# Kernel tuning notes

Hardware: AMD Instinct MI355X
Metric: run time of the kernel (lower is better)

## Reference

```python
import jax, jax.numpy as jnp
import numpy as np

C = 128          # input_channels == output_channels (required by residual + final conv)
MID = C // 4     # hidden width of weight/bias heads
H = W = 64
B = 4
SOFTMAX_SCALE = 1.0


def _leaky(z):
    return jnp.where(z >= 0, z, 0.2 * z)


def _conv1x1(x, w, b):
    # x: [B,Cin,H,W], w: [Cout,Cin], b: [Cout]
    return jnp.einsum('oc,bchw->bohw', w, x) + b[None, :, None, None]


def setup_inputs() -> dict:
    key = jax.random.key(0)
    ks = jax.random.split(key, 16)
    s = 0.05
    inp = {
        'x': jax.random.normal(ks[0], (B, C, H, W), dtype=jnp.float32),
        # 1x1 query / value convs
        'q_w': jax.random.normal(ks[1], (C, C), dtype=jnp.float32) * s,
        'q_b': jnp.zeros((C,), dtype=jnp.float32),
        'v_w': jax.random.normal(ks[2], (C, C), dtype=jnp.float32) * s,
        'v_b': jnp.zeros((C,), dtype=jnp.float32),
        # linear_weight head: conv1x1(C->C/4) -> leaky -> conv1x1(C/4->1)
        'lw1_w': jax.random.normal(ks[3], (MID, C), dtype=jnp.float32) * s,
        'lw1_b': jnp.zeros((MID,), dtype=jnp.float32),
        'lw2_w': jax.random.normal(ks[4], (1, MID), dtype=jnp.float32) * s,
        'lw2_b': jnp.zeros((1,), dtype=jnp.float32),
        # bias head
        'bw1_w': jax.random.normal(ks[5], (MID, C), dtype=jnp.float32) * s,
        'bw1_b': jnp.zeros((MID,), dtype=jnp.float32),
        'bw2_w': jax.random.normal(ks[6], (1, MID), dtype=jnp.float32) * s,
        'bw2_b': jnp.zeros((1,), dtype=jnp.float32),
        # final 3x3 conv (output_channels -> output_channels)
        'lin_w': jax.random.normal(ks[7], (C, C, 3, 3), dtype=jnp.float32) * s,
        'lin_b': jnp.zeros((C,), dtype=jnp.float32),
    }
    return inp


def _attn_sample(q_map, v_map, w_map, b_map):
    # q_map: [C,H,W], v_map: [C,H,W], w_map/b_map: [1,H,W]
    n = H * W
    q = q_map.reshape(C, n)                      # query tokens  [C,N]
    v = v_map.reshape(C, n)                      # value tokens  [C,N]
    w = w_map.reshape(n)
    b = b_map.reshape(n)
    # cosine-normalized keys (normalize each token over channels)
    norm = jnp.sqrt(jnp.sum(q * q, axis=0))      # [N]
    k = q / jnp.clip(norm, 1e-4)[None, :]        # [C,N]
    logits = jnp.einsum('cn,cm->nm', k, q)       # keys x queries [N,N]
    mean = jnp.mean(logits, axis=0, keepdims=True)            # [1,N]
    sparse = jax.nn.relu(logits - mean * w[None, :] + b[None, :])
    mask = (sparse != 0.0).astype(logits.dtype)
    attn = jax.nn.softmax(logits * sparse * SOFTMAX_SCALE, axis=0)
    attn = jnp.clip(attn * mask, 1e-8)
    out = jnp.einsum('cn,nm->cm', v, attn)       # [C,N]
    return out.reshape(C, H, W)


def reference(x, q_w, q_b, v_w, v_b, lw1_w, lw1_b, lw2_w, lw2_b,
              bw1_w, bw1_b, bw2_w, bw2_b, lin_w, lin_b):
    x1 = _conv1x1(x, v_w, v_b)                   # value  [B,C,H,W]
    x2 = _conv1x1(x, q_w, q_b)                   # query  [B,C,H,W]
    weight = _conv1x1(_leaky(_conv1x1(x2, lw1_w, lw1_b)), lw2_w, lw2_b)  # [B,1,H,W]
    bias = _conv1x1(_leaky(_conv1x1(x2, bw1_w, bw1_b)), bw2_w, bw2_b)    # [B,1,H,W]
    y = jax.vmap(_attn_sample)(x2, x1, weight, bias)                      # [B,C,H,W]
    y = jax.lax.conv_general_dilated(
        y, lin_w, window_strides=(1, 1), padding='SAME',
        dimension_numbers=('NCHW', 'OIHW', 'NCHW'))
    y = _leaky(y + lin_b[None, :, None, None])
    return y + x
```

## Files before the change

kernel.cpp:

```cpp
#include <hip/hip_runtime.h>
#include <math.h>

#define BB 4
#define CC 128
#define NN 4096
#define HH 64
#define WW 64
#define YTP 4356

typedef __attribute__((ext_vector_type(8))) short bf16x8;
typedef __attribute__((ext_vector_type(4))) float f32x4;

__device__ inline unsigned short f2bf(float f) {
  unsigned int u = __float_as_uint(f);
  unsigned int r = (u + 0x7FFFu + ((u >> 16) & 1u)) >> 16;
  return (unsigned short)r;
}
__device__ inline float bf2f(short s) {
  union { unsigned u; float f; } x;
  x.u = ((unsigned)(unsigned short)s) << 16;
  return x.f;
}

__global__ __launch_bounds__(256) void xt_kernel(
    const float* __restrict__ x, unsigned short* __restrict__ xtb) {
  int b = blockIdx.y;
  int n0 = blockIdx.x * 64;
  int t = threadIdx.x;
  __shared__ float xs[CC][65];
  for (int l = 0; l < 32; l++) {
    int idx = t + 256 * l;
    int px = idx & 63, c = idx >> 6;
    xs[c][px] = x[((size_t)b * CC + c) * NN + n0 + px];
  }
  __syncthreads();
  int n = t & 63, ch = t >> 6;
  unsigned o[16];
#pragma unroll
  for (int i = 0; i < 32; i += 2) {
    o[i >> 1] = (unsigned)f2bf(xs[32 * ch + i][n]) |
                ((unsigned)f2bf(xs[32 * ch + i + 1][n]) << 16);
  }
  unsigned short* dst = xtb + ((size_t)b * NN + n0 + n) * CC + 32 * ch;
#pragma unroll
  for (int k = 0; k < 4; k++) {
    uint4 v; v.x = o[4 * k]; v.y = o[4 * k + 1]; v.z = o[4 * k + 2]; v.w = o[4 * k + 3];
    *(uint4*)(dst + 8 * k) = v;
  }
}

__global__ __launch_bounds__(256) void wrepack_kernel(
    const float* __restrict__ qw, const float* __restrict__ vw,
    const float* __restrict__ lw1w, const float* __restrict__ bw1w,
    const float* __restrict__ lw, unsigned short* __restrict__ qwb,
    unsigned short* __restrict__ vwb, unsigned short* __restrict__ hwb,
    unsigned short* __restrict__ Wt) {
  int idx = blockIdx.x * 256 + threadIdx.x;
  if (idx < 16384) { qwb[idx] = f2bf(qw[idx]); return; }
  idx -= 16384;
  if (idx < 16384) { vwb[idx] = f2bf(vw[idx]); return; }
  idx -= 16384;
  if (idx < 4096) { hwb[idx] = f2bf(lw1w[idx]); return; }
  idx -= 4096;
  if (idx < 4096) { hwb[4096 + idx] = f2bf(bw1w[idx]); return; }
  idx -= 4096;
  if (idx < CC * 1152) {
    int co = idx / 1152, rem = idx % 1152;
    int tap = rem >> 7, ci = rem & 127;
    Wt[idx] = f2bf(lw[(size_t)(co * CC + ci) * 9 + tap]);
  }
}

__global__ __launch_bounds__(256) void qv_mfma(
    const unsigned short* __restrict__ xtb, const unsigned short* __restrict__ qwb,
    const unsigned short* __restrict__ vwb, const unsigned short* __restrict__ hwb,
    const float* __restrict__ qb, const float* __restrict__ vb,
    const float* __restrict__ lw1b, const float* __restrict__ lw2w,
    const float* __restrict__ lw2b, const float* __restrict__ bw1b,
    const float* __restrict__ bw2w, const float* __restrict__ bw2b,
    unsigned short* __restrict__ qt, unsigned short* __restrict__ qtn,
    float* __restrict__ nrm, float* __restrict__ pSkey,
    unsigned short* __restrict__ vbuf, float* __restrict__ pSumV,
    float* __restrict__ wmap, float* __restrict__ bmap) {
  int b = blockIdx.y;
  int nb = blockIdx.x;
  int n0 = nb * 64;
  int t = threadIdx.x, w = t >> 6, lane = t & 63;
  int col = lane & 15, oct = lane >> 4;
  __shared__ float qs[4][16][132];
  __shared__ float partK[4][128];
  __shared__ float partV[4][128];
  const unsigned short* xb = xtb + (size_t)b * NN * CC;

  f32x4 aq[8], av[8];
#pragma unroll
  for (int i = 0; i < 8; i++) { aq[i] = (f32x4)0.f; av[i] = (f32x4)0.f; }
#pragma unroll
  for (int kc = 0; kc < 4; kc++) {
    bf16x8 Xf = *(const bf16x8*)(xb + (size_t)(n0 + 16 * w + col) * CC + kc * 32 + oct * 8);
#pragma unroll
    for (int ct = 0; ct < 8; ct++) {
      bf16x8 Qf = *(const bf16x8*)(qwb + (16 * ct + col) * CC + kc * 32 + oct * 8);
      aq[ct] = __builtin_amdgcn_mfma_f32_16x16x32_bf16(Xf, Qf, aq[ct], 0, 0, 0);
      bf16x8 Vf = *(const bf16x8*)(vwb + (16 * ct + col) * CC + kc * 32 + oct * 8);
      av[ct] = __builtin_amdgcn_mfma_f32_16x16x32_bf16(Vf, Xf, av[ct], 0, 0, 0);
    }
  }

  unsigned short* vbb = vbuf + (size_t)b * CC * NN;
#pragma unroll
  for (int ct = 0; ct < 8; ct++) {
#pragma unroll
    for (int r = 0; r < 4; r++) {
      int c = 16 * ct + 4 * oct + r;
      float val = av[ct][r] + vb[c];
      vbb[(size_t)c * NN + n0 + 16 * w + col] = f2bf(val);
      float sv = val;
      sv += __shfl_xor(sv, 1); sv += __shfl_xor(sv, 2);
      sv += __shfl_xor(sv, 4); sv += __shfl_xor(sv, 8);
      if (col == 0) partV[w][c] = sv;
    }
  }

#pragma unroll
  for (int ct = 0; ct < 8; ct++) {
#pragma unroll
    for (int r = 0; r < 4; r++) {
      int c = 16 * ct + col;
      qs[w][4 * oct + r][c] = aq[ct][r] + qb[c];
    }
  }
  int row = lane >> 2, cq = (lane & 3) * 32;
  float vals[32];
  float ssq = 0.f;
#pragma unroll
  for (int i = 0; i < 32; i += 4) {
    float4 v4 = *(const float4*)&qs[w][row][cq + i];
    vals[i] = v4.x; vals[i + 1] = v4.y; vals[i + 2] = v4.z; vals[i + 3] = v4.w;
    ssq += v4.x * v4.x + v4.y * v4.y + v4.z * v4.z + v4.w * v4.w;
  }
  ssq += __shfl_xor(ssq, 1); ssq += __shfl_xor(ssq, 2);
  float nm = fmaxf(sqrtf(ssq), 1e-4f), sc = 1.0f / nm;
  int gp = b * NN + n0 + 16 * w + row;
  if ((lane & 3) == 0) nrm[gp] = nm;
  unsigned outq[16], outn[16];
  float sk[32];
#pragma unroll
  for (int i = 0; i < 32; i += 2) {
    unsigned short u0 = f2bf(vals[i]), u1 = f2bf(vals[i + 1]);
    unsigned short m0 = f2bf(vals[i] * sc), m1 = f2bf(vals[i + 1] * sc);
    outq[i >> 1] = (unsigned)u0 | ((unsigned)u1 << 16);
    outn[i >> 1] = (unsigned)m0 | ((unsigned)m1 << 16);
    sk[i] = bf2f((short)m0); sk[i + 1] = bf2f((short)m1);
  }
  unsigned short* qtp = qt + (size_t)gp * CC + cq;
  unsigned short* qnp = qtn + (size_t)gp * CC + cq;
#pragma unroll
  for (int k = 0; k < 4; k++) {
    uint4 v; v.x = outq[4 * k]; v.y = outq[4 * k + 1]; v.z = outq[4 * k + 2]; v.w = outq[4 * k + 3];
    *(uint4*)(qtp + 8 * k) = v;
    uint4 u; u.x = outn[4 * k]; u.y = outn[4 * k + 1]; u.z = outn[4 * k + 2]; u.w = outn[4 * k + 3];
    *(uint4*)(qnp + 8 * k) = u;
  }
#pragma unroll
  for (int i = 0; i < 32; i++) {
    float v = sk[i];
    v += __shfl_xor(v, 4); v += __shfl_xor(v, 8);
    v += __shfl_xor(v, 16); v += __shfl_xor(v, 32);
    if ((lane >> 2) == 0) partK[w][cq + i] = v;
  }

  f32x4 ah[4];
#pragma unroll
  for (int i = 0; i < 4; i++) ah[i] = (f32x4)0.f;
#pragma unroll
  for (int kc = 0; kc < 4; kc++) {
    float4 a0 = *(const float4*)&qs[w][col][kc * 32 + oct * 8];
    float4 a1 = *(const float4*)&qs[w][col][kc * 32 + oct * 8 + 4];
    union { unsigned short s[8]; bf16x8 v; } af;
    af.s[0] = f2bf(a0.x); af.s[1] = f2bf(a0.y); af.s[2] = f2bf(a0.z); af.s[3] = f2bf(a0.w);
    af.s[4] = f2bf(a1.x); af.s[5] = f2bf(a1.y); af.s[6] = f2bf(a1.z); af.s[7] = f2bf(a1.w);
#pragma unroll
    for (int ct = 0; ct < 4; ct++) {
      bf16x8 Bf = *(const bf16x8*)(hwb + (16 * ct + col) * CC + kc * 32 + oct * 8);
      ah[ct] = __builtin_amdgcn_mfma_f32_16x16x32_bf16(af.v, Bf, ah[ct], 0, 0, 0);
    }
  }
  float b1l[2], b1b[2], w2l[2], w2b[2];
#pragma unroll
  for (int ct = 0; ct < 2; ct++) {
    int mid = 16 * ct + col;
    b1l[ct] = lw1b[mid]; w2l[ct] = lw2w[mid];
    b1b[ct] = bw1b[mid]; w2b[ct] = bw2w[mid];
  }
#pragma unroll
  for (int r = 0; r < 4; r++) {
    float wp = 0.f, bp = 0.f;
#pragma unroll
    for (int ct = 0; ct < 2; ct++) {
      float zl = ah[ct][r] + b1l[ct];
      zl = (zl >= 0.f) ? zl : 0.2f * zl;
      wp += w2l[ct] * zl;
      float zb = ah[ct + 2][r] + b1b[ct];
      zb = (zb >= 0.f) ? zb : 0.2f * zb;
      bp += w2b[ct] * zb;
    }
    wp += __shfl_xor(wp, 1); wp += __shfl_xor(wp, 2);
    wp += __shfl_xor(wp, 4); wp += __shfl_xor(wp, 8);
    bp += __shfl_xor(bp, 1); bp += __shfl_xor(bp, 2);
    bp += __shfl_xor(bp, 4); bp += __shfl_xor(bp, 8);
    if (col == 0) {
      int g = b * NN + n0 + 16 * w + 4 * oct + r;
      wmap[g] = wp + lw2b[0];
      bmap[g] = bp + bw2b[0];
    }
  }

  __syncthreads();
  int blk = b * 64 + nb;
  if (t < 128) {
    float s = (partK[0][t] + partK[1][t]) + (partK[2][t] + partK[3][t]);
    pSkey[(size_t)blk * 128 + t] = s;
  } else {
    int c = t - 128;
    float s = (partV[0][c] + partV[1][c]) + (partV[2][c] + partV[3][c]);
    pSumV[(size_t)blk * 128 + c] = s;
  }
}

__global__ __launch_bounds__(256) void reduce_kernel(
    const float* __restrict__ pSkey, const float* __restrict__ pSumV,
    float* __restrict__ Skey, float* __restrict__ SumV) {
  int b = blockIdx.x;
  int t = threadIdx.x;
  const float* src = (t < 128) ? pSkey : pSumV;
  int c = t & 127;
  float s = 0.f;
#pragma unroll 8
  for (int nb = 0; nb < 64; nb++)
    s += src[((size_t)b * 64 + nb) * 128 + c];
  if (t < 128) Skey[b * CC + c] = s;
  else SumV[b * CC + c] = s;
}

__global__ __launch_bounds__(256, 2) void qk_sparse(
    const unsigned short* __restrict__ qt, const unsigned short* __restrict__ qtn,
    const float* __restrict__ nrm, const float* __restrict__ wmap,
    const float* __restrict__ bmap, const float* __restrict__ Skey,
    float* __restrict__ Zacc, unsigned short* __restrict__ Tb,
    int* __restrict__ blist, int* __restrict__ bcnt) {
  int lin = blockIdx.x;
  int mtile = lin >> 6;
  int bks = lin & 63;
  int b = bks >> 4, ks = bks & 15;
  int t = threadIdx.x, wave = t >> 6, lane = t & 63;
  int col = lane & 15, oct = lane >> 4;
  int m0 = mtile * 128 + 32 * wave;
  int bucket = b * 128 + (m0 >> 5);

  __shared__ unsigned short Bt[2][4096];
  __shared__ unsigned short tS[4][32][40];

  const unsigned short* qtb  = qt  + (size_t)b * NN * CC;
  const unsigned short* qtnb = qtn + (size_t)b * NN * CC;

  bf16x8 A[2][4];
#pragma unroll
  for (int mt = 0; mt < 2; mt++)
#pragma unroll
    for (int kc = 0; kc < 4; kc++)
      A[mt][kc] = *(const bf16x8*)(qtb + (size_t)(m0 + 16 * mt + col) * CC + 32 * kc + 8 * oct);

  float stc1[2][4], stzd[2][4];
#pragma unroll
  for (int mt = 0; mt < 2; mt++) {
    float dot = 0.f;
#pragma unroll
    for (int kc = 0; kc < 4; kc++) {
      const float* skp = Skey + b * CC + 32 * kc + 8 * oct;
      float4 s0 = *(const float4*)skp;
      float4 s1 = *(const float4*)(skp + 4);
      bf16x8 a = A[mt][kc];
      dot += bf2f(a[0]) * s0.x + bf2f(a[1]) * s0.y + bf2f(a[2]) * s0.z + bf2f(a[3]) * s0.w;
      dot += bf2f(a[4]) * s1.x + bf2f(a[5]) * s1.y + bf2f(a[6]) * s1.z + bf2f(a[7]) * s1.w;
    }
    dot += __shfl_xor(dot, 16);
    dot += __shfl_xor(dot, 32);
    int m = m0 + 16 * mt + col;
    float c1 = dot * (1.0f / NN) * wmap[(size_t)b * NN + m] - bmap[(size_t)b * NN + m];
    float nm = nrm[(size_t)b * NN + m];
    float zd = nm * fmaxf(nm - c1, 0.f);
#pragma unroll
    for (int r = 0; r < 4; r++) {
      stc1[mt][r] = __shfl(c1, 4 * oct + r);
      stzd[mt][r] = __shfl(zd, 4 * oct + r);
    }
  }

  int n0base = ks * 256;
  {
    int f0 = wave, f1 = wave + 4;
    uint4 r0 = *(const uint4*)(qtnb + (size_t)(n0base + 16 * (f0 >> 2) + col) * CC + (4 * (f0 & 3) + oct) * 8);
    uint4 r1 = *(const uint4*)(qtnb + (size_t)(n0base + 16 * (f1 >> 2) + col) * CC + (4 * (f1 & 3) + oct) * 8);
    *(uint4*)&Bt[0][f0 * 512 + lane * 8] = r0;
    *(uint4*)&Bt[0][f1 * 512 + lane * 8] = r1;
  }
  __syncthreads();

  float zp[2][4];
#pragma unroll
  for (int mt = 0; mt < 2; mt++)
#pragma unroll
    for (int r = 0; r < 4; r++) zp[mt][r] = 0.f;
  bool didwork = false;

  for (int it = 0; it < 8; it++) {
    int cur = it & 1;
    bool more = (it + 1 < 8);
    uint4 r0, r1;
    if (more) {
      int n0n = n0base + (it + 1) * 32;
      int f0 = wave, f1 = wave + 4;
      r0 = *(const uint4*)(qtnb + (size_t)(n0n + 16 * (f0 >> 2) + col) * CC + (4 * (f0 & 3) + oct) * 8);
      r1 = *(const uint4*)(qtnb + (size_t)(n0n + 16 * (f1 >> 2) + col) * CC + (4 * (f1 & 3) + oct) * 8);
    }
    f32x4 acc[2][2];
    acc[0][0] = (f32x4)0.f; acc[0][1] = (f32x4)0.f;
    acc[1][0] = (f32x4)0.f; acc[1][1] = (f32x4)0.f;
#pragma unroll
    for (int nt = 0; nt < 2; nt++)
#pragma unroll
      for (int kc = 0; kc < 4; kc++) {
        bf16x8 Bf = *(const bf16x8*)&Bt[cur][(nt * 4 + kc) * 512 + lane * 8];
        acc[0][nt] = __builtin_amdgcn_mfma_f32_16x16x32_bf16(A[0][kc], Bf, acc[0][nt], 0, 0, 0);
        acc[1][nt] = __builtin_amdgcn_mfma_f32_16x16x32_bf16(A[1][kc], Bf, acc[1][nt], 0, 0, 0);
      }
    float fm = -1e30f;
#pragma unroll
    for (int mt = 0; mt < 2; mt++)
#pragma unroll
      for (int r = 0; r < 4; r++) {
        float lm = fmaxf(acc[mt][0][r], acc[mt][1][r]);
        float ub = fmaxf(lm * fmaxf(lm - stc1[mt][r], 0.f), 0.f);
        fm = fmaxf(fm, ub - stzd[mt][r]);
      }
    if (__any(fm > -18.4207f)) {
      didwork = true;
      int n0 = n0base + it * 32;
#pragma unroll
      for (int mt = 0; mt < 2; mt++)
#pragma unroll
        for (int nt = 0; nt < 2; nt++)
#pragma unroll
          for (int r = 0; r < 4; r++) {
            float l = acc[mt][nt][r];
            float s = l - stc1[mt][r];
            float z = l * fmaxf(s, 0.f);
            float e = __expf(z - stzd[mt][r]);
            zp[mt][r] += e;
            tS[wave][16 * mt + 4 * oct + r][16 * nt + col] = f2bf((s > 0.f) ? e : 0.f);
          }
      int idx;
      if (lane == 0) {
        idx = atomicAdd(&bcnt[bucket], 1);
        if (idx < 128) blist[bucket * 128 + idx] = n0 >> 5;
      }
      idx = __shfl(idx, 0);
      if (idx < 128) {
        const unsigned short* src = &tS[wave][lane >> 1][(lane & 1) * 16];
        unsigned short* dst = Tb + ((size_t)bucket * 128 + idx) * 1024 +
                              (lane >> 1) * 32 + (lane & 1) * 16;
        *(uint4*)dst = *(const uint4*)src;
        *(uint4*)(dst + 8) = *(const uint4*)(src + 8);
      }
    }
    if (more) {
      int nxt = cur ^ 1;
      *(uint4*)&Bt[nxt][wave * 512 + lane * 8] = r0;
      *(uint4*)&Bt[nxt][(wave + 4) * 512 + lane * 8] = r1;
    }
    __syncthreads();
  }

  if (didwork) {
#pragma unroll
    for (int mt = 0; mt < 2; mt++)
#pragma unroll
      for (int r = 0; r < 4; r++) {
        float v = zp[mt][r];
        v += __shfl_xor(v, 1); v += __shfl_xor(v, 2);
        v += __shfl_xor(v, 4); v += __shfl_xor(v, 8);
        if (col == 0)
          atomicAdd(Zacc + (size_t)b * NN + m0 + 16 * mt + 4 * oct + r, v);
      }
  }
}

__global__ __launch_bounds__(1024, 1) void pv_kernel(
    const unsigned short* __restrict__ vb16, const unsigned short* __restrict__ Tb,
    const int* __restrict__ blist, const int* __restrict__ bcnt,
    const float* __restrict__ Zacc, const float* __restrict__ SumV,
    unsigned short* __restrict__ Yt) {
  int bucket = blockIdx.x;
  int b = bucket >> 7;
  int m0 = (bucket & 127) * 32;
  int t = threadIdx.x;
  int w = t >> 6, lane = t & 63;
  int grp = w >> 2, cw = w & 3;
  int col = lane & 15, oct = lane >> 4;
  __shared__ int lst[128];
  __shared__ float red[3][32][132];
  int ntiles = bcnt[bucket];
  if (ntiles > 128) ntiles = 128;
  if (t < ntiles) lst[t] = blist[bucket * 128 + t];
  __syncthreads();
  const unsigned short* Vb = vb16 + (size_t)b * CC * NN;
  const unsigned short* Tbb = Tb + (size_t)bucket * 128 * 1024;

  f32x4 acc[2][2];
  acc[0][0] = (f32x4)0.f; acc[0][1] = (f32x4)0.f;
  acc[1][0] = (f32x4)0.f; acc[1][1] = (f32x4)0.f;

  int nIt = (ntiles > grp) ? ((ntiles - grp + 3) >> 2) : 0;
  bf16x8 B0a, B0b, A0a, A0b, B1a, B1b, A1a, A1b;
  auto ld0 = [&](int idx) {
    int n0 = lst[idx] * 32;
    const unsigned short* Tp = Tbb + (size_t)idx * 1024;
    B0a = *(const bf16x8*)(Tp + col * 32 + 8 * oct);
    B0b = *(const bf16x8*)(Tp + (16 + col) * 32 + 8 * oct);
    A0a = *(const bf16x8*)(Vb + (size_t)(32 * cw + col) * NN + n0 + 8 * oct);
    A0b = *(const bf16x8*)(Vb + (size_t)(32 * cw + 16 + col) * NN + n0 + 8 * oct);
  };
  auto ld1 = [&](int idx) {
    int n0 = lst[idx] * 32;
    const unsigned short* Tp = Tbb + (size_t)idx * 1024;
    B1a = *(const bf16x8*)(Tp + col * 32 + 8 * oct);
    B1b = *(const bf16x8*)(Tp + (16 + col) * 32 + 8 * oct);
    A1a = *(const bf16x8*)(Vb + (size_t)(32 * cw + col) * NN + n0 + 8 * oct);
    A1b = *(const bf16x8*)(Vb + (size_t)(32 * cw + 16 + col) * NN + n0 + 8 * oct);
  };
  if (nIt > 0) ld0(grp);
  for (int k = 0; k < nIt; k += 2) {
    if (k + 1 < nIt) ld1(grp + (k + 1) * 4);
    acc[0][0] = __builtin_amdgcn_mfma_f32_16x16x32_bf16(A0a, B0a, acc[0][0], 0, 0, 0);
    acc[0][1] = __builtin_amdgcn_mfma_f32_16x16x32_bf16(A0a, B0b, acc[0][1], 0, 0, 0);
    acc[1][0] = __builtin_amdgcn_mfma_f32_16x16x32_bf16(A0b, B0a, acc[1][0], 0, 0, 0);
    acc[1][1] = __builtin_amdgcn_mfma_f32_16x16x32_bf16(A0b, B0b, acc[1][1], 0, 0, 0);
    if (k + 1 < nIt) {
      if (k + 2 < nIt) ld0(grp + (k + 2) * 4);
      acc[0][0] = __builtin_amdgcn_mfma_f32_16x16x32_bf16(A1a, B1a, acc[0][0], 0, 0, 0);
      acc[0][1] = __builtin_amdgcn_mfma_f32_16x16x32_bf16(A1a, B1b, acc[0][1], 0, 0, 0);
      acc[1][0] = __builtin_amdgcn_mfma_f32_16x16x32_bf16(A1b, B1a, acc[1][0], 0, 0, 0);
      acc[1][1] = __builtin_amdgcn_mfma_f32_16x16x32_bf16(A1b, B1b, acc[1][1], 0, 0, 0);
    }
  }

  if (grp > 0) {
#pragma unroll
    for (int bt = 0; bt < 2; bt++)
#pragma unroll
      for (int ct = 0; ct < 2; ct++)
#pragma unroll
        for (int r = 0; r < 4; r++)
          red[grp - 1][16 * bt + col][32 * cw + 16 * ct + 4 * oct + r] = acc[ct][bt][r];
  }
  __syncthreads();
  if (grp == 0) {
#pragma unroll
    for (int bt = 0; bt < 2; bt++) {
      int m = m0 + 16 * bt + col;
      float rZ = 1.0f / Zacc[(size_t)b * NN + m];
      int h = m >> 6, ww = m & 63;
      unsigned short* yp = Yt + ((size_t)b * YTP + (size_t)(h + 1) * 66 + (ww + 1)) * CC + 32 * cw;
#pragma unroll
      for (int ct = 0; ct < 2; ct++) {
        int cbase = 16 * ct + 4 * oct;
        float4 sv = *(const float4*)(SumV + b * CC + 32 * cw + cbase);
        float y[4];
#pragma unroll
        for (int r = 0; r < 4; r++) {
          float a = acc[ct][bt][r]
                  + red[0][16 * bt + col][32 * cw + cbase + r]
                  + red[1][16 * bt + col][32 * cw + cbase + r]
                  + red[2][16 * bt + col][32 * cw + cbase + r];
          y[r] = a * rZ;
        }
        y[0] += 1e-8f * sv.x; y[1] += 1e-8f * sv.y;
        y[2] += 1e-8f * sv.z; y[3] += 1e-8f * sv.w;
        uint2 o;
        o.x = (unsigned)f2bf(y[0]) | ((unsigned)f2bf(y[1]) << 16);
        o.y = (unsigned)f2bf(y[2]) | ((unsigned)f2bf(y[3]) << 16);
        *(uint2*)(yp + cbase) = o;
      }
    }
  }
}

__global__ __launch_bounds__(256, 2) void conv_mfma(
    const unsigned short* __restrict__ Yt, const unsigned short* __restrict__ Wt,
    const float* __restrict__ x, const float* __restrict__ lb,
    float* __restrict__ out) {
  int h = blockIdx.x;
  int by = blockIdx.y;
  int b = blockIdx.z;
  int t = threadIdx.x;
  int wave = t >> 6, lane = t & 63;
  int col = lane & 15, oct = lane >> 4;
  int pxt = wave & 1, cohalf = wave >> 1;
  int w0 = by * 32 + pxt * 16;
  const unsigned short* Yb = Yt + (size_t)b * YTP * CC;

  f32x4 acc[4];
#pragma unroll
  for (int ct = 0; ct < 4; ct++) acc[ct] = (f32x4)0.f;

#pragma unroll
  for (int tap = 0; tap < 9; tap++) {
    int dh = tap / 3 - 1, dw = tap % 3 - 1;
    const unsigned short* ybase =
        Yb + (size_t)((h + 1 + dh) * 66 + (w0 + 1 + dw + col)) * CC;
#pragma unroll
    for (int kc = 0; kc < 4; kc++) {
      bf16x8 Af = *(const bf16x8*)(ybase + 32 * kc + 8 * oct);
#pragma unroll
      for (int ct = 0; ct < 4; ct++) {
        bf16x8 Bf = *(const bf16x8*)(Wt +
            (size_t)(cohalf * 64 + 16 * ct + col) * 1152 + tap * 128 + 32 * kc + 8 * oct);
        acc[ct] = __builtin_amdgcn_mfma_f32_16x16x32_bf16(Af, Bf, acc[ct], 0, 0, 0);
      }
    }
  }
#pragma unroll
  for (int ct = 0; ct < 4; ct++) {
    int co = cohalf * 64 + 16 * ct + col;
    float bv = lb[co];
    int n = h * 64 + w0 + 4 * oct;
    size_t base = ((size_t)b * CC + co) * NN + n;
    float4 xi = *(const float4*)(x + base);
    float4 o;
    float z0 = acc[ct][0] + bv; o.x = ((z0 >= 0.f) ? z0 : 0.2f * z0) + xi.x;
    float z1 = acc[ct][1] + bv; o.y = ((z1 >= 0.f) ? z1 : 0.2f * z1) + xi.y;
    float z2 = acc[ct][2] + bv; o.z = ((z2 >= 0.f) ? z2 : 0.2f * z2) + xi.z;
    float z3 = acc[ct][3] + bv; o.w = ((z3 >= 0.f) ? z3 : 0.2f * z3) + xi.w;
    *(float4*)(out + base) = o;
  }
}

extern "C" void kernel_launch(void* const* d_in, const int* in_sizes, int n_in,
                              void* d_out, int out_size, void* d_ws, size_t ws_size,
                              hipStream_t stream) {
  const float* x    = (const float*)d_in[0];
  const float* q_w  = (const float*)d_in[1];
  const float* q_b  = (const float*)d_in[2];
  const float* v_w  = (const float*)d_in[3];
  const float* v_b  = (const float*)d_in[4];
  const float* lw1w = (const float*)d_in[5];
  const float* lw1b = (const float*)d_in[6];
  const float* lw2w = (const float*)d_in[7];
  const float* lw2b = (const float*)d_in[8];
  const float* bw1w = (const float*)d_in[9];
  const float* bw1b = (const float*)d_in[10];
  const float* bw2w = (const float*)d_in[11];
  const float* bw2b = (const float*)d_in[12];
  const float* linw = (const float*)d_in[13];
  const float* linb = (const float*)d_in[14];
  float* out = (float*)d_out;

  const size_t BCN = (size_t)BB * CC * NN;
  const size_t BN  = (size_t)BB * NN;

  unsigned short* xtb = (unsigned short*)d_ws;
  unsigned short* qt  = xtb + BCN;
  unsigned short* qtn = qt + BCN;
  unsigned short* vb16 = qtn + BCN;
  unsigned short* Yt  = vb16 + BCN;
  unsigned short* qwb = Yt + (size_t)BB * YTP * CC;
  unsigned short* vwb = qwb + CC * CC;
  unsigned short* hwb = vwb + CC * CC;
  unsigned short* Wt  = hwb + 64 * CC;
  float* nrmb = (float*)(Wt + (size_t)CC * 1152);
  float* wmap = nrmb + BN;
  float* bmap = wmap + BN;
  float* SumV = bmap + BN;
  float* Skey = SumV + (size_t)BB * CC;
  float* Zacc = Skey + (size_t)BB * CC;
  int*   cnt  = (int*)(Zacc + BN);
  int*   bcnt = cnt + 16;
  float* pSkey = (float*)(bcnt + 512);
  float* pSumV = pSkey + 256 * 128;
  int*   blist = (int*)(pSumV + 256 * 128);
  unsigned short* Tb = (unsigned short*)(blist + 512 * 128);

  hipMemsetAsync(Zacc, 0, BN * sizeof(float) + (16 + 512) * sizeof(int), stream);
  hipMemsetAsync(Yt, 0, (size_t)BB * YTP * CC * sizeof(unsigned short), stream);

  hipLaunchKernelGGL(xt_kernel, dim3(NN / 64, BB), dim3(256), 0, stream, x, xtb);
  hipLaunchKernelGGL(wrepack_kernel, dim3((188416 + 255) / 256), dim3(256), 0,
                     stream, q_w, v_w, lw1w, bw1w, linw, qwb, vwb, hwb, Wt);
  hipLaunchKernelGGL(qv_mfma, dim3(NN / 64, BB), dim3(256), 0, stream,
                     xtb, qwb, vwb, hwb, q_b, v_b, lw1b, lw2w, lw2b,
                     bw1b, bw2w, bw2b, qt, qtn, nrmb, pSkey, vb16, pSumV,
                     wmap, bmap);
  hipLaunchKernelGGL(reduce_kernel, dim3(BB), dim3(256), 0, stream,
                     pSkey, pSumV, Skey, SumV);
  hipLaunchKernelGGL(qk_sparse, dim3(2048), dim3(256), 0, stream,
                     qt, qtn, nrmb, wmap, bmap, Skey, Zacc, Tb, blist, bcnt);
  hipLaunchKernelGGL(pv_kernel, dim3(512), dim3(1024), 0, stream,
                     vb16, Tb, blist, bcnt, Zacc, SumV, Yt);
  hipLaunchKernelGGL(conv_mfma, dim3(HH, 2, BB), dim3(256), 0, stream,
                     Yt, Wt, x, linb, out);
}
```

Before: 249.6 us.

## Split PV reduction across tile chunks with fp32 atomic accumulation and finalize kernel

The PV stage now splits each query bucket's key-tile list into chunks of 16 tiles over a second grid dimension, so up to 8 blocks work on one bucket instead of one block looping over all tiles. Partial results are atomically added into a new fp32 Yacc buffer, and a separate yfin kernel applies the 1/Z normalization and SumV term and writes the padded bf16 Yt. The aim is to spread uneven sparse work across more CUs and cut per-block serial latency. The cost is a larger memset (the fp32 accumulator), many global atomics, an extra kernel launch, and loss of the software-pipelined loads.

```diff
diff --git a/kernel.cpp b/kernel.cpp
--- a/kernel.cpp
+++ b/kernel.cpp
@@ -399,101 +399,111 @@
 __global__ __launch_bounds__(1024, 1) void pv_kernel(
     const unsigned short* __restrict__ vb16, const unsigned short* __restrict__ Tb,
     const int* __restrict__ blist, const int* __restrict__ bcnt,
-    const float* __restrict__ Zacc, const float* __restrict__ SumV,
-    unsigned short* __restrict__ Yt) {
+    const unsigned short* __restrict__ zeroT,
+    float* __restrict__ Yacc) {
+  int bucket = blockIdx.y;
+  int chunk = blockIdx.x;
+  int ntiles = bcnt[bucket];
+  if (ntiles > 128) ntiles = 128;
+  if (chunk * 16 >= ntiles) return;
+  int b = bucket >> 7;
+  int t = threadIdx.x;
+  int w = t >> 6, lane = t & 63;
+  int grp = w >> 2, cw = w & 3;
+  int col = lane & 15, oct = lane >> 4;
+  __shared__ float red[3][32][132];
+
+  const unsigned short* Vb = vb16 + (size_t)b * CC * NN;
+  const unsigned short* Tbb = Tb + (size_t)bucket * 128 * 1024;
+  const int* bl = blist + bucket * 128;
+
+  int n0s[4];
+  const unsigned short* Tps[4];
+  int base = chunk * 16 + grp;
+#pragma unroll
+  for (int j = 0; j < 4; j++) {
+    int idx = base + 4 * j;
+    bool ok = idx < ntiles;
+    n0s[j] = ok ? bl[idx] * 32 : 0;
+    Tps[j] = ok ? (Tbb + (size_t)idx * 1024) : zeroT;
+  }
+
+  f32x4 acc[2][2];
+  acc[0][0] = (f32x4)0.f; acc[0][1] = (f32x4)0.f;
+  acc[1][0] = (f32x4)0.f; acc[1][1] = (f32x4)0.f;
+
+#pragma unroll
+  for (int j = 0; j < 4; j++) {
+    bf16x8 Ba = *(const bf16x8*)(Tps[j] + col * 32 + 8 * oct);
+    bf16x8 Bb = *(const bf16x8*)(Tps[j] + (16 + col) * 32 + 8 * oct);
+    bf16x8 Aa = *(const bf16x8*)(Vb + (size_t)(32 * cw + col) * NN + n0s[j] + 8 * oct);
+    bf16x8 Ab = *(const bf16x8*)(Vb + (size_t)(32 * cw + 16 + col) * NN + n0s[j] + 8 * oct);
+    acc[0][0] = __builtin_amdgcn_mfma_f32_16x16x32_bf16(Aa, Ba, acc[0][0], 0, 0, 0);
+    acc[0][1] = __builtin_amdgcn_mfma_f32_16x16x32_bf16(Aa, Bb, acc[0][1], 0, 0, 0);
+    acc[1][0] = __builtin_amdgcn_mfma_f32_16x16x32_bf16(Ab, Ba, acc[1][0], 0, 0, 0);
+    acc[1][1] = __builtin_amdgcn_mfma_f32_16x16x32_bf16(Ab, Bb, acc[1][1], 0, 0, 0);
+  }
+
+  if (grp > 0) {
+#pragma unroll
+    for (int bt = 0; bt < 2; bt++)
+#pragma unroll
+      for (int ct = 0; ct < 2; ct++)
+#pragma unroll
+        for (int r = 0; r < 4; r++)
+          red[grp - 1][16 * bt + col][32 * cw + 16 * ct + 4 * oct + r] = acc[ct][bt][r];
+  }
+  __syncthreads();
+  if (grp == 0) {
+#pragma unroll
+    for (int bt = 0; bt < 2; bt++) {
+      int m = (bucket & 127) * 32 + 16 * bt + col;
+#pragma unroll
+      for (int ct = 0; ct < 2; ct++) {
+        int cbase = 32 * cw + 16 * ct + 4 * oct;
+#pragma unroll
+        for (int r = 0; r < 4; r++) {
+          float a = acc[ct][bt][r]
+                  + red[0][16 * bt + col][cbase + r]
+                  + red[1][16 * bt + col][cbase + r]
+                  + red[2][16 * bt + col][cbase + r];
+          atomicAdd(Yacc + ((size_t)(b * NN + m)) * CC + cbase + r, a);
+        }
+      }
+    }
+  }
+}
+
+__global__ __launch_bounds__(256) void yfin_kernel(
+    const float* __restrict__ Yacc, const float* __restrict__ Zacc,
+    const float* __restrict__ SumV, unsigned short* __restrict__ Yt) {
   int bucket = blockIdx.x;
   int b = bucket >> 7;
   int m0 = (bucket & 127) * 32;
   int t = threadIdx.x;
-  int w = t >> 6, lane = t & 63;
-  int grp = w >> 2, cw = w & 3;
-  int col = lane & 15, oct = lane >> 4;
-  __shared__ int lst[128];
-  __shared__ float red[3][32][132];
-  int ntiles = bcnt[bucket];
-  if (ntiles > 128) ntiles = 128;
-  if (t < ntiles) lst[t] = blist[bucket * 128 + t];
-  __syncthreads();
-  const unsigned short* Vb = vb16 + (size_t)b * CC * NN;
-  const unsigned short* Tbb = Tb + (size_t)bucket * 128 * 1024;
-
-  f32x4 acc[2][2];
-  acc[0][0] = (f32x4)0.f; acc[0][1] = (f32x4)0.f;
-  acc[1][0] = (f32x4)0.f; acc[1][1] = (f32x4)0.f;
-
-  int nIt = (ntiles > grp) ? ((ntiles - grp + 3) >> 2) : 0;
-  bf16x8 B0a, B0b, A0a, A0b, B1a, B1b, A1a, A1b;
-  auto ld0 = [&](int idx) {
-    int n0 = lst[idx] * 32;
-    const unsigned short* Tp = Tbb + (size_t)idx * 1024;
-    B0a = *(const bf16x8*)(Tp + col * 32 + 8 * oct);
-    B0b = *(const bf16x8*)(Tp + (16 + col) * 32 + 8 * oct);
-    A0a = *(const bf16x8*)(Vb + (size_t)(32 * cw + col) * NN + n0 + 8 * oct);
-    A0b = *(const bf16x8*)(Vb + (size_t)(32 * cw + 16 + col) * NN + n0 + 8 * oct);
-  };
-  auto ld1 = [&](int idx) {
-    int n0 = lst[idx] * 32;
-    const unsigned short* Tp = Tbb + (size_t)idx * 1024;
-    B1a = *(const bf16x8*)(Tp + col * 32 + 8 * oct);
-    B1b = *(const bf16x8*)(Tp + (16 + col) * 32 + 8 * oct);
-    A1a = *(const bf16x8*)(Vb + (size_t)(32 * cw + col) * NN + n0 + 8 * oct);
-    A1b = *(const bf16x8*)(Vb + (size_t)(32 * cw + 16 + col) * NN + n0 + 8 * oct);
-  };
-  if (nIt > 0) ld0(grp);
-  for (int k = 0; k < nIt; k += 2) {
-    if (k + 1 < nIt) ld1(grp + (k + 1) * 4);
-    acc[0][0] = __builtin_amdgcn_mfma_f32_16x16x32_bf16(A0a, B0a, acc[0][0], 0, 0, 0);
-    acc[0][1] = __builtin_amdgcn_mfma_f32_16x16x32_bf16(A0a, B0b, acc[0][1], 0, 0, 0);
-    acc[1][0] = __builtin_amdgcn_mfma_f32_16x16x32_bf16(A0b, B0a, acc[1][0], 0, 0, 0);
-    acc[1][1] = __builtin_amdgcn_mfma_f32_16x16x32_bf16(A0b, B0b, acc[1][1], 0, 0, 0);
-    if (k + 1 < nIt) {
-      if (k + 2 < nIt) ld0(grp + (k + 2) * 4);
-      acc[0][0] = __builtin_amdgcn_mfma_f32_16x16x32_bf16(A1a, B1a, acc[0][0], 0, 0, 0);
-      acc[0][1] = __builtin_amdgcn_mfma_f32_16x16x32_bf16(A1a, B1b, acc[0][1], 0, 0, 0);
-      acc[1][0] = __builtin_amdgcn_mfma_f32_16x16x32_bf16(A1b, B1a, acc[1][0], 0, 0, 0);
-      acc[1][1] = __builtin_amdgcn_mfma_f32_16x16x32_bf16(A1b, B1b, acc[1][1], 0, 0, 0);
-    }
-  }
-
-  if (grp > 0) {
-#pragma unroll
-    for (int bt = 0; bt < 2; bt++)
-#pragma unroll
-      for (int ct = 0; ct < 2; ct++)
-#pragma unroll
-        for (int r = 0; r < 4; r++)
-          red[grp - 1][16 * bt + col][32 * cw + 16 * ct + 4 * oct + r] = acc[ct][bt][r];
-  }
-  __syncthreads();
-  if (grp == 0) {
-#pragma unroll
-    for (int bt = 0; bt < 2; bt++) {
-      int m = m0 + 16 * bt + col;
-      float rZ = 1.0f / Zacc[(size_t)b * NN + m];
-      int h = m >> 6, ww = m & 63;
-      unsigned short* yp = Yt + ((size_t)b * YTP + (size_t)(h + 1) * 66 + (ww + 1)) * CC + 32 * cw;
-#pragma unroll
-      for (int ct = 0; ct < 2; ct++) {
-        int cbase = 16 * ct + 4 * oct;
-        float4 sv = *(const float4*)(SumV + b * CC + 32 * cw + cbase);
-        float y[4];
-#pragma unroll
-        for (int r = 0; r < 4; r++) {
-          float a = acc[ct][bt][r]
-                  + red[0][16 * bt + col][32 * cw + cbase + r]
-                  + red[1][16 * bt + col][32 * cw + cbase + r]
-                  + red[2][16 * bt + col][32 * cw + cbase + r];
-          y[r] = a * rZ;
-        }
-        y[0] += 1e-8f * sv.x; y[1] += 1e-8f * sv.y;
-        y[2] += 1e-8f * sv.z; y[3] += 1e-8f * sv.w;
-        uint2 o;
-        o.x = (unsigned)f2bf(y[0]) | ((unsigned)f2bf(y[1]) << 16);
-        o.y = (unsigned)f2bf(y[2]) | ((unsigned)f2bf(y[3]) << 16);
-        *(uint2*)(yp + cbase) = o;
-      }
-    }
-  }
+  int mi = t >> 3, c0 = (t & 7) * 16;
+  int m = m0 + mi;
+  float rZ = 1.0f / Zacc[(size_t)b * NN + m];
+  int h = m >> 6, ww = m & 63;
+  const float* ya = Yacc + ((size_t)(b * NN + m)) * CC + c0;
+  const float* sv = SumV + b * CC + c0;
+  unsigned short* yp = Yt + ((size_t)b * YTP + (size_t)(h + 1) * 66 + (ww + 1)) * CC + c0;
+  unsigned ov[8];
+#pragma unroll
+  for (int j = 0; j < 4; j++) {
+    float4 a = *(const float4*)(ya + 4 * j);
+    float4 s = *(const float4*)(sv + 4 * j);
+    float y0 = a.x * rZ + 1e-8f * s.x;
+    float y1 = a.y * rZ + 1e-8f * s.y;
+    float y2 = a.z * rZ + 1e-8f * s.z;
+    float y3 = a.w * rZ + 1e-8f * s.w;
+    ov[2 * j]     = (unsigned)f2bf(y0) | ((unsigned)f2bf(y1) << 16);
+    ov[2 * j + 1] = (unsigned)f2bf(y2) | ((unsigned)f2bf(y3) << 16);
+  }
+  uint4 o0; o0.x = ov[0]; o0.y = ov[1]; o0.z = ov[2]; o0.w = ov[3];
+  uint4 o1; o1.x = ov[4]; o1.y = ov[5]; o1.z = ov[6]; o1.w = ov[7];
+  *(uint4*)yp = o0;
+  *(uint4*)(yp + 8) = o1;
 }
 
 __global__ __launch_bounds__(256, 2) void conv_mfma(
@@ -586,12 +596,17 @@
   float* Zacc = Skey + (size_t)BB * CC;
   int*   cnt  = (int*)(Zacc + BN);
   int*   bcnt = cnt + 16;
-  float* pSkey = (float*)(bcnt + 512);
+  unsigned short* zeroT = (unsigned short*)(bcnt + 512);
+  float* Yacc = (float*)(zeroT + 1024);
+  float* pSkey = Yacc + (size_t)BN * CC;
   float* pSumV = pSkey + 256 * 128;
   int*   blist = (int*)(pSumV + 256 * 128);
   unsigned short* Tb = (unsigned short*)(blist + 512 * 128);
 
-  hipMemsetAsync(Zacc, 0, BN * sizeof(float) + (16 + 512) * sizeof(int), stream);
+  size_t zbytes = BN * sizeof(float) + (16 + 512) * sizeof(int) +
+                  1024 * sizeof(unsigned short) +
+                  (size_t)BN * CC * sizeof(float);
+  hipMemsetAsync(Zacc, 0, zbytes, stream);
   hipMemsetAsync(Yt, 0, (size_t)BB * YTP * CC * sizeof(unsigned short), stream);
 
   hipLaunchKernelGGL(xt_kernel, dim3(NN / 64, BB), dim3(256), 0, stream, x, xtb);
@@ -605,8 +620,10 @@
                      pSkey, pSumV, Skey, SumV);
   hipLaunchKernelGGL(qk_sparse, dim3(2048), dim3(256), 0, stream,
                      qt, qtn, nrmb, wmap, bmap, Skey, Zacc, Tb, blist, bcnt);
-  hipLaunchKernelGGL(pv_kernel, dim3(512), dim3(1024), 0, stream,
-                     vb16, Tb, blist, bcnt, Zacc, SumV, Yt);
+  hipLaunchKernelGGL(pv_kernel, dim3(8, 512), dim3(1024), 0, stream,
+                     vb16, Tb, blist, bcnt, zeroT, Yacc);
+  hipLaunchKernelGGL(yfin_kernel, dim3(512), dim3(256), 0, stream,
+                     Yacc, Zacc, SumV, Yt);
   hipLaunchKernelGGL(conv_mfma, dim3(HH, 2, BB), dim3(256), 0, stream,
                      Yt, Wt, x, linb, out);
 }
```

Measured after the change: 325.1 us. 30.2% more time.
